# Kernel tuning notes

Hardware: AMD Instinct MI355X
Metric: run time of the kernel (lower is better)

## Reference

```python
import jax, jax.numpy as jnp
import numpy as np

# Module constants (kernels_desc / kernels_radius from the PA-Seg GatedCRF config)
RADIUS = (3, 3, 1)          # kernels_radius per (H, W, D)
SIGMA_XY = 5.0              # sigma for the spatial 'xy' mesh feature
SIGMA_IMG = 0.1             # sigma for the image intensity feature
WEIGHT = 1.0                # kernel weight


def _unfold(img, radius):
    """NCHWD -> (N, C, kH, kW, kD, H*W*D) sliding windows, zero-padded (matches unfoldNd)."""
    N, C, H, W, D = img.shape
    kH, kW, kD = (2 * radius[0] + 1, 2 * radius[1] + 1, 2 * radius[2] + 1)
    patches = jax.lax.conv_general_dilated_patches(
        img, (kH, kW, kD), (1, 1, 1),
        [(radius[0], radius[0]), (radius[1], radius[1]), (radius[2], radius[2])])
    # output channel dim is C-major over (C, kH, kW, kD)
    return patches.reshape(N, C, kH, kW, kD, H * W * D)


def _get_mesh(N, H, W, D, spacing, dtype):
    # spacing: (3, N) physical voxel spacings per axis per volume
    ah = jnp.arange(H, dtype=dtype)[None, :, None, None]
    aw = jnp.arange(W, dtype=dtype)[None, None, :, None]
    ad = jnp.arange(D, dtype=dtype)[None, None, None, :]
    sH = spacing[0][:, None, None, None]
    sW = spacing[1][:, None, None, None]
    sD = spacing[2][:, None, None, None]
    mh = jnp.broadcast_to(sH * ah, (N, H, W, D))
    mw = jnp.broadcast_to(sW * aw, (N, H, W, D))
    md = jnp.broadcast_to(sD * ad, (N, H, W, D))
    return jnp.stack([mh, mw, md], axis=1)  # (N, 3, H, W, D)


def _create_kernels(sample, spacing, N, H, W, D):
    mesh = _get_mesh(N, H, W, D, spacing, sample.dtype) / SIGMA_XY
    feats = jnp.concatenate([mesh, sample / SIGMA_IMG], axis=1)  # (N, 4, H, W, D)
    rH, rW, rD = RADIUS
    f_unf = _unfold(feats, RADIUS)                                # (N, 4, kH, kW, kD, L)
    center = f_unf[:, :, rH, rW, rD, :][:, :, None, None, None, :]
    k = jnp.exp((-0.5 * (f_unf - center) ** 2).sum(axis=1, keepdims=True))
    k = k.at[:, :, rH, rW, rD, :].set(0.0)
    return WEIGHT * k                                             # (N, 1, kH, kW, kD, L)


def setup_inputs() -> dict:
    key = jax.random.key(0)
    k1, k2, k3 = jax.random.split(key, 3)
    N, C, H, W, D = 1, 2, 64, 64, 32
    logits = jax.random.normal(k1, (N, C, H, W, D), dtype=jnp.float32)
    y_hat_softmax = jax.nn.softmax(logits, axis=1)
    sample = jax.random.normal(k2, (N, 1, H, W, D), dtype=jnp.float32)
    spacing = jax.random.uniform(k3, (3, N), dtype=jnp.float32, minval=0.5, maxval=2.0)
    return {"y_hat_softmax": y_hat_softmax, "sample": sample, "spacing": spacing}


def reference(y_hat_softmax, sample, spacing):
    N, C, H, W, D = y_hat_softmax.shape
    kernels = _create_kernels(sample, spacing, N, H, W, D)        # (N,1,kH,kW,kD,L)
    y_unf = _unfold(y_hat_softmax, RADIUS)                        # (N,C,kH,kW,kD,L)
    prod = (kernels * y_unf).sum(axis=(2, 3, 4))                  # (N, C, L)
    prod = prod.reshape(N, C, H, W, D)
    loss = kernels.sum() - (prod * y_hat_softmax).sum()
    denom = N * H * W * D
    return loss / denom
```

## Files before the change

kernel.cpp:

```cpp
#include <hip/hip_runtime.h>

#define NH 64
#define NW 64
#define ND 32
#define LTOT (NH * NW * ND)


__global__ __launch_bounds__(256, 4)
void gatedcrf3d_kernel(const float* __restrict__ y,
                       const float* __restrict__ sample,
                       const float* __restrict__ spacing,
                       float* __restrict__ out)
{
    constexpr int cDH[24] = {0,0,0, 1,1,1,1,1,1,1, 2,2,2,2,2,2,2, 3,3,3,3,3,3,3};
    constexpr int cDW[24] = {1,2,3, -3,-2,-1,0,1,2,3, -3,-2,-1,0,1,2,3, -3,-2,-1,0,1,2,3};

    const int tid = threadIdx.x;
    const int sub = tid >> 7;
    const int p   = blockIdx.x * 128 + (tid & 127);

    const int d = p & (ND - 1);
    const int w = (p >> 5) & (NW - 1);
    const int h = p >> 11;

    const float sH = spacing[0] * 0.2f;
    const float sW = spacing[1] * 0.2f;
    const float sD = spacing[2] * 0.2f;
    const float nh2 = -0.5f * sH * sH;
    const float nw2 = -0.5f * sW * sW;
    const float nd2 = -0.5f * sD * sD;

    const float ic  = sample[p] * 10.0f;
    const float y0c = y[p];
    const float y1c = y[LTOT + p];

    float acc   = 0.0f;
    float extra = 0.0f;

    auto pair_body = [&](int dh, int dw) {
        const int hh = h + dh;
        const int ww = w + dw;
        const bool ibhw = ((unsigned)hh < NH) & ((unsigned)ww < NW);
        const int hc = min(max(hh, 0), NH - 1);
        const int wc = min(max(ww, 0), NW - 1);
        const int qb = (hc << 11) + (wc << 5);
        const float spatHW = nh2 * (float)(dh * dh) + nw2 * (float)(dw * dw);
        #pragma unroll
        for (int dd = -1; dd <= 1; ++dd) {
            const int zz = d + dd;
            const bool inb = ibhw & ((unsigned)zz < ND);
            const int zc = min(max(zz, 0), ND - 1);
            const int q = qb + zc;
            const float sq  = sample[q];
            const float y0q = y[q];
            const float y1q = y[LTOT + q];
            const float di  = __builtin_fmaf(sq, 10.0f, -ic);
            const float spat = (dd == 0) ? spatHW : (spatHW + nd2);
            const float arg  = __builtin_fmaf(di, -0.5f * di, spat);
            const float k    = __expf(arg);
            const float t    = 1.0f - __builtin_fmaf(y0q, y0c, y1q * y1c);
            acc += inb ? (k * t) : 0.0f;
        }
    };

    if (sub == 0) {
        #pragma unroll
        for (int i = 0; i < 24; i += 2) pair_body(cDH[i], cDW[i]);
        {
            const int zz = d + 1;
            const bool inb = zz < ND;
            const int q = (h << 11) + (w << 5) + (inb ? zz : d);
            const float di  = __builtin_fmaf(sample[q], 10.0f, -ic);
            const float arg = __builtin_fmaf(di, -0.5f * di, nd2);
            const float k   = __expf(arg);
            const float t   = 1.0f - __builtin_fmaf(y[q], y0c, y[LTOT + q] * y1c);
            acc += inb ? (k * t) : 0.0f;
        }
    } else {
        #pragma unroll
        for (int i = 1; i < 24; i += 2) pair_body(cDH[i], cDW[i]);
        {
            const int nhv = min(h, 3) + min(NH - 1 - h, 3) + 1;
            const int nwv = min(w, 3) + min(NW - 1 - w, 3) + 1;
            const int ndv = min(d, 1) + min(ND - 1 - d, 1) + 1;
            const int cnt = 147 - nhv * nwv * ndv;
            const float argo = nh2 * (float)(h * h) + nw2 * (float)(w * w)
                             + nd2 * (float)(d * d) + (-0.5f) * ic * ic;
            extra = (float)cnt * __expf(argo);
        }
    }

    float contrib = __builtin_fmaf(2.0f, acc, extra);

    #pragma unroll
    for (int off = 32; off > 0; off >>= 1)
        contrib += __shfl_down(contrib, off, 64);

    __shared__ float red[4];
    if ((tid & 63) == 0) red[tid >> 6] = contrib;
    __syncthreads();
    if (tid == 0) {
        atomicAdd(out, (red[0] + red[1] + red[2] + red[3]) * (1.0f / (float)LTOT));
    }
}

extern "C" void kernel_launch(void* const* d_in, const int* in_sizes, int n_in,
                              void* d_out, int out_size, void* d_ws, size_t ws_size,
                              hipStream_t stream) {
    const float* y       = (const float*)d_in[0];
    const float* sample  = (const float*)d_in[1];
    const float* spacing = (const float*)d_in[2];
    float* out = (float*)d_out;

    hipMemsetAsync(out, 0, sizeof(float), stream);

    const int threads = 256;
    const int blocks = LTOT / 128;
    gatedcrf3d_kernel<<<blocks, threads, 0, stream>>>(y, sample, spacing, out);
}
```

Measured before the change: 74.94 us.

## Pack inputs into interleaved float4 workspace and split neighbor pairs across eight waves

```diff
diff --git a/kernel.cpp b/kernel.cpp
--- a/kernel.cpp
+++ b/kernel.cpp
@@ -6,18 +6,22 @@
 #define LTOT (NH * NW * ND)
 
 
-__global__ __launch_bounds__(256, 4)
-void gatedcrf3d_kernel(const float* __restrict__ y,
-                       const float* __restrict__ sample,
+__global__ __launch_bounds__(256)
+void pack_kernel(const float* __restrict__ y, const float* __restrict__ sample,
+                 float4* __restrict__ ws4)
+{
+    const int p = blockIdx.x * 256 + threadIdx.x;
+    ws4[p] = make_float4(y[p], y[LTOT + p], sample[p] * 10.0f, 0.0f);
+}
+
+__global__ __launch_bounds__(512, 4)
+void gatedcrf3d_kernel(const float4* __restrict__ ws4,
                        const float* __restrict__ spacing,
                        float* __restrict__ out)
 {
-    constexpr int cDH[24] = {0,0,0, 1,1,1,1,1,1,1, 2,2,2,2,2,2,2, 3,3,3,3,3,3,3};
-    constexpr int cDW[24] = {1,2,3, -3,-2,-1,0,1,2,3, -3,-2,-1,0,1,2,3, -3,-2,-1,0,1,2,3};
-
     const int tid = threadIdx.x;
-    const int sub = tid >> 7;
-    const int p   = blockIdx.x * 128 + (tid & 127);
+    const int sub = tid >> 6;
+    const int p   = blockIdx.x * 64 + (tid & 63);
 
     const int d = p & (ND - 1);
     const int w = (p >> 5) & (NW - 1);
@@ -30,9 +34,8 @@
     const float nw2 = -0.5f * sW * sW;
     const float nd2 = -0.5f * sD * sD;
 
-    const float ic  = sample[p] * 10.0f;
-    const float y0c = y[p];
-    const float y1c = y[LTOT + p];
+    const float4 c = ws4[p];
+    const float y0c = c.x, y1c = c.y, ic = c.z;
 
     float acc   = 0.0f;
     float extra = 0.0f;
@@ -50,44 +53,44 @@
             const int zz = d + dd;
             const bool inb = ibhw & ((unsigned)zz < ND);
             const int zc = min(max(zz, 0), ND - 1);
-            const int q = qb + zc;
-            const float sq  = sample[q];
-            const float y0q = y[q];
-            const float y1q = y[LTOT + q];
-            const float di  = __builtin_fmaf(sq, 10.0f, -ic);
+            const float4 f = ws4[qb + zc];
+            const float di = f.z - ic;
             const float spat = (dd == 0) ? spatHW : (spatHW + nd2);
             const float arg  = __builtin_fmaf(di, -0.5f * di, spat);
             const float k    = __expf(arg);
-            const float t    = 1.0f - __builtin_fmaf(y0q, y0c, y1q * y1c);
+            const float t    = 1.0f - __builtin_fmaf(f.x, y0c, f.y * y1c);
             acc += inb ? (k * t) : 0.0f;
         }
     };
 
+    const int base = sub * 3;
+    #pragma unroll
+    for (int j = 0; j < 3; ++j) {
+        const int idx = base + j;
+        int dh, dw;
+        if (idx < 3) { dh = 0; dw = idx + 1; }
+        else { const int t = idx - 3; dh = 1 + t / 7; dw = t % 7 - 3; }
+        pair_body(dh, dw);
+    }
+
     if (sub == 0) {
-        #pragma unroll
-        for (int i = 0; i < 24; i += 2) pair_body(cDH[i], cDW[i]);
-        {
-            const int zz = d + 1;
-            const bool inb = zz < ND;
-            const int q = (h << 11) + (w << 5) + (inb ? zz : d);
-            const float di  = __builtin_fmaf(sample[q], 10.0f, -ic);
-            const float arg = __builtin_fmaf(di, -0.5f * di, nd2);
-            const float k   = __expf(arg);
-            const float t   = 1.0f - __builtin_fmaf(y[q], y0c, y[LTOT + q] * y1c);
-            acc += inb ? (k * t) : 0.0f;
-        }
-    } else {
-        #pragma unroll
-        for (int i = 1; i < 24; i += 2) pair_body(cDH[i], cDW[i]);
-        {
-            const int nhv = min(h, 3) + min(NH - 1 - h, 3) + 1;
-            const int nwv = min(w, 3) + min(NW - 1 - w, 3) + 1;
-            const int ndv = min(d, 1) + min(ND - 1 - d, 1) + 1;
-            const int cnt = 147 - nhv * nwv * ndv;
-            const float argo = nh2 * (float)(h * h) + nw2 * (float)(w * w)
-                             + nd2 * (float)(d * d) + (-0.5f) * ic * ic;
-            extra = (float)cnt * __expf(argo);
-        }
+        const int zz = d + 1;
+        const bool inb = zz < ND;
+        const int q = (h << 11) + (w << 5) + (inb ? zz : d);
+        const float4 f = ws4[q];
+        const float di  = f.z - ic;
+        const float arg = __builtin_fmaf(di, -0.5f * di, nd2);
+        const float k   = __expf(arg);
+        const float t   = 1.0f - __builtin_fmaf(f.x, y0c, f.y * y1c);
+        acc += inb ? (k * t) : 0.0f;
+    } else if (sub == 7) {
+        const int nhv = min(h, 3) + min(NH - 1 - h, 3) + 1;
+        const int nwv = min(w, 3) + min(NW - 1 - w, 3) + 1;
+        const int ndv = min(d, 1) + min(ND - 1 - d, 1) + 1;
+        const int cnt = 147 - nhv * nwv * ndv;
+        const float argo = nh2 * (float)(h * h) + nw2 * (float)(w * w)
+                         + nd2 * (float)(d * d) - 0.5f * ic * ic;
+        extra = (float)cnt * __expf(argo);
     }
 
     float contrib = __builtin_fmaf(2.0f, acc, extra);
@@ -96,11 +99,13 @@
     for (int off = 32; off > 0; off >>= 1)
         contrib += __shfl_down(contrib, off, 64);
 
-    __shared__ float red[4];
+    __shared__ float red[8];
     if ((tid & 63) == 0) red[tid >> 6] = contrib;
     __syncthreads();
     if (tid == 0) {
-        atomicAdd(out, (red[0] + red[1] + red[2] + red[3]) * (1.0f / (float)LTOT));
+        const float s = red[0] + red[1] + red[2] + red[3]
+                      + red[4] + red[5] + red[6] + red[7];
+        atomicAdd(out, s * (1.0f / (float)LTOT));
     }
 }
 
@@ -111,10 +116,10 @@
     const float* sample  = (const float*)d_in[1];
     const float* spacing = (const float*)d_in[2];
     float* out = (float*)d_out;
+    float4* ws4 = (float4*)d_ws;
 
     hipMemsetAsync(out, 0, sizeof(float), stream);
 
-    const int threads = 256;
-    const int blocks = LTOT / 128;
-    gatedcrf3d_kernel<<<blocks, threads, 0, stream>>>(y, sample, spacing, out);
+    pack_kernel<<<LTOT / 256, 256, 0, stream>>>(y, sample, ws4);
+    gatedcrf3d_kernel<<<LTOT / 64, 512, 0, stream>>>(ws4, spacing, out);
 }
```

New measurement: 88.65 us. 18.3% more time.

## Split neighbor work across 8 sub-groups per voxel with 1024-thread blocks

Applied to the files above, without the earlier changes.

```diff
diff --git a/kernel.cpp b/kernel.cpp
--- a/kernel.cpp
+++ b/kernel.cpp
@@ -6,88 +6,100 @@
 #define LTOT (NH * NW * ND)
 
 
-__global__ __launch_bounds__(256, 4)
+__global__ __launch_bounds__(1024, 8)
 void gatedcrf3d_kernel(const float* __restrict__ y,
                        const float* __restrict__ sample,
                        const float* __restrict__ spacing,
                        float* __restrict__ out)
 {
-    constexpr int cDH[24] = {0,0,0, 1,1,1,1,1,1,1, 2,2,2,2,2,2,2, 3,3,3,3,3,3,3};
-    constexpr int cDW[24] = {1,2,3, -3,-2,-1,0,1,2,3, -3,-2,-1,0,1,2,3, -3,-2,-1,0,1,2,3};
-
     const int tid = threadIdx.x;
     const int sub = tid >> 7;
-    const int p   = blockIdx.x * 128 + (tid & 127);
+    const int v   = tid & 127;
 
-    const int d = p & (ND - 1);
-    const int w = (p >> 5) & (NW - 1);
-    const int h = p >> 11;
+    const int h = blockIdx.x >> 4;
+    const int w = ((blockIdx.x & 15) << 2) + (v >> 5);
+    const int d = v & 31;
+    const int p = (h << 11) + (w << 5) + d;
+
+    constexpr float L2E  = 1.4426950408889634f;
+    constexpr float NHL2 = -0.5f * L2E;
 
     const float sH = spacing[0] * 0.2f;
     const float sW = spacing[1] * 0.2f;
     const float sD = spacing[2] * 0.2f;
-    const float nh2 = -0.5f * sH * sH;
-    const float nw2 = -0.5f * sW * sW;
-    const float nd2 = -0.5f * sD * sD;
+    const float nh2 = NHL2 * sH * sH;
+    const float nw2 = NHL2 * sW * sW;
+    const float nd2 = NHL2 * sD * sD;
 
     const float ic  = sample[p] * 10.0f;
     const float y0c = y[p];
     const float y1c = y[LTOT + p];
 
-    float acc   = 0.0f;
-    float extra = 0.0f;
+    const int  zm = max(d - 1, 0);
+    const int  zp = min(d + 1, ND - 1);
+    const bool vm = d > 0;
+    const bool vp = d < ND - 1;
 
-    auto pair_body = [&](int dh, int dw) {
+    float acc = 0.0f, extra = 0.0f;
+
+    auto PB = [&](int dh, int dw) {
         const int hh = h + dh;
         const int ww = w + dw;
-        const bool ibhw = ((unsigned)hh < NH) & ((unsigned)ww < NW);
-        const int hc = min(max(hh, 0), NH - 1);
+        const bool ibhw = (hh < NH) & ((unsigned)ww < NW);
+        const int hc = min(hh, NH - 1);
         const int wc = min(max(ww, 0), NW - 1);
         const int qb = (hc << 11) + (wc << 5);
-        const float spatHW = nh2 * (float)(dh * dh) + nw2 * (float)(dw * dw);
-        #pragma unroll
-        for (int dd = -1; dd <= 1; ++dd) {
-            const int zz = d + dd;
-            const bool inb = ibhw & ((unsigned)zz < ND);
-            const int zc = min(max(zz, 0), ND - 1);
-            const int q = qb + zc;
-            const float sq  = sample[q];
-            const float y0q = y[q];
-            const float y1q = y[LTOT + q];
-            const float di  = __builtin_fmaf(sq, 10.0f, -ic);
-            const float spat = (dd == 0) ? spatHW : (spatHW + nd2);
-            const float arg  = __builtin_fmaf(di, -0.5f * di, spat);
-            const float k    = __expf(arg);
-            const float t    = 1.0f - __builtin_fmaf(y0q, y0c, y1q * y1c);
-            acc += inb ? (k * t) : 0.0f;
-        }
+        const float spat0 = nh2 * (float)(dh * dh) + nw2 * (float)(dw * dw);
+        const float spat1 = spat0 + nd2;
+        const int q0 = qb + zm, q1 = qb + d, q2 = qb + zp;
+        const float s0 = sample[q0], s1 = sample[q1], s2 = sample[q2];
+        const float a0 = y[q0],      a1 = y[q1],      a2 = y[q2];
+        const float b0 = y[LTOT+q0], b1 = y[LTOT+q1], b2 = y[LTOT+q2];
+
+        float di, arg, k, t;
+        di  = __builtin_fmaf(s0, 10.0f, -ic);
+        arg = __builtin_fmaf(di * NHL2, di, spat1);
+        k   = __builtin_exp2f(arg);
+        t   = 1.0f - __builtin_fmaf(a0, y0c, b0 * y1c);
+        acc += (ibhw & vm) ? k * t : 0.0f;
+
+        di  = __builtin_fmaf(s1, 10.0f, -ic);
+        arg = __builtin_fmaf(di * NHL2, di, spat0);
+        k   = __builtin_exp2f(arg);
+        t   = 1.0f - __builtin_fmaf(a1, y0c, b1 * y1c);
+        acc += ibhw ? k * t : 0.0f;
+
+        di  = __builtin_fmaf(s2, 10.0f, -ic);
+        arg = __builtin_fmaf(di * NHL2, di, spat1);
+        k   = __builtin_exp2f(arg);
+        t   = 1.0f - __builtin_fmaf(a2, y0c, b2 * y1c);
+        acc += (ibhw & vp) ? k * t : 0.0f;
     };
 
-    if (sub == 0) {
-        #pragma unroll
-        for (int i = 0; i < 24; i += 2) pair_body(cDH[i], cDW[i]);
-        {
-            const int zz = d + 1;
-            const bool inb = zz < ND;
-            const int q = (h << 11) + (w << 5) + (inb ? zz : d);
+    switch (sub) {
+      case 0: PB(0,1); PB(0,2); PB(0,3); {
+            const int q = (h << 11) + (w << 5) + zp;
             const float di  = __builtin_fmaf(sample[q], 10.0f, -ic);
-            const float arg = __builtin_fmaf(di, -0.5f * di, nd2);
-            const float k   = __expf(arg);
+            const float arg = __builtin_fmaf(di * NHL2, di, nd2);
+            const float k   = __builtin_exp2f(arg);
             const float t   = 1.0f - __builtin_fmaf(y[q], y0c, y[LTOT + q] * y1c);
-            acc += inb ? (k * t) : 0.0f;
-        }
-    } else {
-        #pragma unroll
-        for (int i = 1; i < 24; i += 2) pair_body(cDH[i], cDW[i]);
-        {
+            acc += vp ? k * t : 0.0f;
+        } break;
+      case 1: PB(1,-3); PB(1,-2); PB(1,-1); break;
+      case 2: PB(1, 0); PB(1, 1); PB(1, 2); break;
+      case 3: PB(1, 3); PB(2,-3); PB(2,-2); break;
+      case 4: PB(2,-1); PB(2, 0); PB(2, 1); break;
+      case 5: PB(2, 2); PB(2, 3); PB(3,-3); break;
+      case 6: PB(3,-2); PB(3,-1); PB(3, 0); break;
+      case 7: PB(3, 1); PB(3, 2); PB(3, 3); {
             const int nhv = min(h, 3) + min(NH - 1 - h, 3) + 1;
             const int nwv = min(w, 3) + min(NW - 1 - w, 3) + 1;
             const int ndv = min(d, 1) + min(ND - 1 - d, 1) + 1;
             const int cnt = 147 - nhv * nwv * ndv;
             const float argo = nh2 * (float)(h * h) + nw2 * (float)(w * w)
-                             + nd2 * (float)(d * d) + (-0.5f) * ic * ic;
-            extra = (float)cnt * __expf(argo);
-        }
+                             + nd2 * (float)(d * d) + NHL2 * ic * ic;
+            extra = (float)cnt * __builtin_exp2f(argo);
+        } break;
     }
 
     float contrib = __builtin_fmaf(2.0f, acc, extra);
@@ -96,11 +108,14 @@
     for (int off = 32; off > 0; off >>= 1)
         contrib += __shfl_down(contrib, off, 64);
 
-    __shared__ float red[4];
+    __shared__ float red[16];
     if ((tid & 63) == 0) red[tid >> 6] = contrib;
     __syncthreads();
     if (tid == 0) {
-        atomicAdd(out, (red[0] + red[1] + red[2] + red[3]) * (1.0f / (float)LTOT));
+        float s = 0.0f;
+        #pragma unroll
+        for (int i = 0; i < 16; ++i) s += red[i];
+        atomicAdd(out, s * (1.0f / (float)LTOT));
     }
 }
 
@@ -114,7 +129,5 @@
 
     hipMemsetAsync(out, 0, sizeof(float), stream);
 
-    const int threads = 256;
-    const int blocks = LTOT / 128;
-    gatedcrf3d_kernel<<<blocks, threads, 0, stream>>>(y, sample, spacing, out);
+    gatedcrf3d_kernel<<<LTOT / 128, 1024, 0, stream>>>(y, sample, spacing, out);
 }
```

Measured after the change: 74.25 us. Within noise of the previous version (-0.9%).
